# Kernel tuning notes

Measured on AMD Instinct MI355X. Metric: run time of the kernel, lower is better.

Reference implementation:

```python
import jax, jax.numpy as jnp
import numpy as np

D_MODEL = 1024
N_HEADS = 16
D_HEAD = 64
NUM_REL_POS = 2047
B = 8
L = 1024


def setup_inputs() -> dict:
    key = jax.random.key(0)
    ks = jax.random.split(key, 8)
    s = 1.0 / np.sqrt(D_MODEL)
    x = jax.random.normal(ks[0], (B, L, D_MODEL), dtype=jnp.float32)
    rel_indices = jax.random.randint(ks[1], (L, L), 0, NUM_REL_POS)
    Wq = jax.random.normal(ks[2], (D_MODEL, D_MODEL), dtype=jnp.float32) * s
    Wk = jax.random.normal(ks[3], (D_MODEL, D_MODEL), dtype=jnp.float32) * s
    Wv = jax.random.normal(ks[4], (D_MODEL, D_MODEL), dtype=jnp.float32) * s
    Wo = jax.random.normal(ks[5], (D_MODEL, D_MODEL), dtype=jnp.float32) * s
    rel_k = jax.random.normal(ks[6], (NUM_REL_POS, D_HEAD), dtype=jnp.float32) * 0.02
    rel_v = jax.random.normal(ks[7], (NUM_REL_POS, D_HEAD), dtype=jnp.float32) * 0.02
    return {"x": x, "rel_indices": rel_indices, "Wq": Wq, "Wk": Wk,
            "Wv": Wv, "Wo": Wo, "rel_k": rel_k, "rel_v": rel_v}


def reference(x, rel_indices, Wq, Wk, Wv, Wo, rel_k, rel_v):
    Bz, Ls, D = x.shape
    H, dk = N_HEADS, D_HEAD
    scale = 1.0 / np.sqrt(dk)
    # torch Linear: y = x @ W.T, weights are [out, in]
    q = jnp.einsum('bld,ed->ble', x, Wq).reshape(Bz, Ls, H, dk).transpose(0, 2, 1, 3)
    k = jnp.einsum('bld,ed->ble', x, Wk).reshape(Bz, Ls, H, dk).transpose(0, 2, 1, 3)
    v = jnp.einsum('bld,ed->ble', x, Wv).reshape(Bz, Ls, H, dk).transpose(0, 2, 1, 3)
    r_k = rel_k[rel_indices]  # (L, L, dk)
    r_v = rel_v[rel_indices]  # (L, L, dk)
    content = jnp.einsum('bhid,bhjd->bhij', q, k)
    rel = jnp.einsum('bhid,ijd->bhij', q, r_k)
    scores = (content + rel) * scale
    probs = jax.nn.softmax(scores, axis=-1)  # dropout = 0 (eval)
    out = jnp.einsum('bhij,bhjd->bhid', probs, v) + jnp.einsum('bhij,ijd->bhid', probs, r_v)
    out = out.transpose(0, 2, 1, 3).reshape(Bz, Ls, D)
    return jnp.einsum('bld,ed->ble', out, Wo)
```

## Files before the change

kernel.cpp:

```cpp
#include <hip/hip_runtime.h>

#define B_ 8
#define H_ 16
#define L_ 1024
#define DH_ 64
#define DM_ 1024
#define NP_ 2047
#define NP2_ 2048
#define SCALE_ 0.125f

#define PS_ 1032
#define HS_ 260

typedef __attribute__((ext_vector_type(8))) short bf16x8;
typedef __attribute__((ext_vector_type(4))) float f32x4;

__device__ __forceinline__ unsigned short f2bf(float x) {
    union { float f; unsigned int u; } v; v.f = x;
    return (unsigned short)((v.u + 0x7FFFu + ((v.u >> 16) & 1u)) >> 16);
}
__device__ __forceinline__ float bf2f(unsigned short b) {
    union { unsigned int u; float f; } v; v.u = ((unsigned int)b) << 16;
    return v.f;
}

template <int MODE>
__global__ __launch_bounds__(256) void proj_gemm(const float* __restrict__ X,
                                                 const float* __restrict__ W,
                                                 float* __restrict__ Yf,
                                                 unsigned short* __restrict__ Y0,
                                                 unsigned short* __restrict__ Y1)
{
    __shared__ __align__(16) float As[16][132];
    __shared__ __align__(16) float Bs[16][132];
    const int t   = threadIdx.x;
    const int tm  = t & 15;
    const int tn  = t >> 4;
    const int row0 = blockIdx.x * 128;
    const int col0 = blockIdx.y * 128;
    const int lr  = t >> 1;
    const int lc  = (t & 1) * 8;

    float acc[8][8];
#pragma unroll
    for (int i = 0; i < 8; ++i)
#pragma unroll
        for (int j = 0; j < 8; ++j) acc[i][j] = 0.f;

    float4 xa, xb, wa, wb;
    const float* xp = X + (size_t)(row0 + lr) * DM_ + lc;
    const float* wp = W + (size_t)(col0 + lr) * DM_ + lc;
    xa = *(const float4*)(xp);     xb = *(const float4*)(xp + 4);
    wa = *(const float4*)(wp);     wb = *(const float4*)(wp + 4);

    for (int k0 = 0; k0 < DM_; k0 += 16) {
        __syncthreads();
        As[lc + 0][lr] = xa.x; As[lc + 1][lr] = xa.y; As[lc + 2][lr] = xa.z; As[lc + 3][lr] = xa.w;
        As[lc + 4][lr] = xb.x; As[lc + 5][lr] = xb.y; As[lc + 6][lr] = xb.z; As[lc + 7][lr] = xb.w;
        Bs[lc + 0][lr] = wa.x; Bs[lc + 1][lr] = wa.y; Bs[lc + 2][lr] = wa.z; Bs[lc + 3][lr] = wa.w;
        Bs[lc + 4][lr] = wb.x; Bs[lc + 5][lr] = wb.y; Bs[lc + 6][lr] = wb.z; Bs[lc + 7][lr] = wb.w;
        __syncthreads();
        if (k0 + 16 < DM_) {
            xa = *(const float4*)(xp + k0 + 16);  xb = *(const float4*)(xp + k0 + 20);
            wa = *(const float4*)(wp + k0 + 16);  wb = *(const float4*)(wp + k0 + 20);
        }
#pragma unroll
        for (int kk = 0; kk < 16; ++kk) {
            float4 a0 = *(const float4*)&As[kk][tm * 4];
            float4 a1 = *(const float4*)&As[kk][64 + tm * 4];
            float4 b0 = *(const float4*)&Bs[kk][tn * 8];
            float4 b1 = *(const float4*)&Bs[kk][tn * 8 + 4];
            const float av[8] = {a0.x, a0.y, a0.z, a0.w, a1.x, a1.y, a1.z, a1.w};
            const float bv[8] = {b0.x, b0.y, b0.z, b0.w, b1.x, b1.y, b1.z, b1.w};
#pragma unroll
            for (int i = 0; i < 8; ++i)
#pragma unroll
                for (int j = 0; j < 8; ++j)
                    acc[i][j] = fmaf(av[i], bv[j], acc[i][j]);
        }
    }

    const int bidx = row0 >> 10;
    const int hbase = blockIdx.y * 2 + (tn >> 3);
    const int dbase = (tn & 7) * 8;

    if constexpr (MODE == 1) {
#pragma unroll
        for (int i = 0; i < 8; ++i) {
            const int row = row0 + ((i < 4) ? (tm * 4 + i) : (64 + tm * 4 + i - 4));
            *(float4*)(Yf + (size_t)row * DM_ + col0 + tn * 8)     = make_float4(acc[i][0], acc[i][1], acc[i][2], acc[i][3]);
            *(float4*)(Yf + (size_t)row * DM_ + col0 + tn * 8 + 4) = make_float4(acc[i][4], acc[i][5], acc[i][6], acc[i][7]);
        }
    }
    if constexpr (MODE == 0) {
#pragma unroll
        for (int i = 0; i < 8; ++i) {
            const int row = row0 + ((i < 4) ? (tm * 4 + i) : (64 + tm * 4 + i - 4));
            const int l = row & 1023;
            const size_t base = (((size_t)bidx * H_ + hbase) * L_ + l) * DH_ + dbase;
#pragma unroll
            for (int jh = 0; jh < 2; ++jh) {
                ushort4 hi4, lo4;
                unsigned short* hp = (unsigned short*)&hi4;
                unsigned short* lp = (unsigned short*)&lo4;
#pragma unroll
                for (int j = 0; j < 4; ++j) {
                    const float y = acc[i][jh * 4 + j];
                    unsigned short hb = f2bf(y);
                    hp[j] = hb;
                    lp[j] = f2bf(y - bf2f(hb));
                }
                *(ushort4*)(Y0 + base + jh * 4) = hi4;
                *(ushort4*)(Y1 + base + jh * 4) = lo4;
            }
        }
    }
    if constexpr (MODE == 2) {
#pragma unroll
        for (int j = 0; j < 8; ++j) {
            const int d = dbase + j;
            const size_t cb = ((size_t)(bidx * H_ + hbase) * DH_ + d) * L_;
#pragma unroll
            for (int half = 0; half < 2; ++half) {
                const int l0 = (row0 & 1023) + half * 64 + tm * 4;
                ushort4 v4;
                unsigned short* vp = (unsigned short*)&v4;
#pragma unroll
                for (int i = 0; i < 4; ++i) vp[i] = f2bf(acc[half * 4 + i][j]);
                *(ushort4*)(Y0 + cb + l0) = v4;
            }
        }
    }
}

__global__ __launch_bounds__(256) void prep_rel(const float* __restrict__ rk,
                                                const float* __restrict__ rv,
                                                unsigned short* __restrict__ rk_hi,
                                                unsigned short* __restrict__ rv_t)
{
    const int idx = blockIdx.x * 256 + threadIdx.x;
    const int p = idx >> 6;
    const int d = idx & 63;
    float xk = (p < NP_) ? rk[(size_t)p * DH_ + d] : 0.f;
    rk_hi[idx] = f2bf(xk);
    float xv = (p < NP_) ? rv[(size_t)p * DH_ + d] : 0.f;
    rv_t[(size_t)d * NP2_ + p] = f2bf(xv);
}

__global__ __launch_bounds__(512, 4) void shaw_attn_mfma(
    const unsigned short* __restrict__ qh, const unsigned short* __restrict__ ql,
    const unsigned short* __restrict__ kh, const unsigned short* __restrict__ kl,
    const unsigned short* __restrict__ vt, const int* __restrict__ ridx,
    const unsigned short* __restrict__ rkh, const unsigned short* __restrict__ rvt,
    float* __restrict__ out)
{
    __shared__ __align__(16) unsigned char regionA[16 * PS_ * 2];
    __shared__ __align__(16) unsigned char regionB[16 * HS_ * 4];
    __shared__ float pmax[16][8];
    __shared__ float psum[16][8];

    char*           qrel8 = (char*)regionA;
    unsigned short* Pu    = (unsigned short*)regionA;
    float*          hist  = (float*)regionB;
    float*          red   = (float*)regionB;

    const int t    = threadIdx.x;
    const int w    = t >> 6;
    const int lane = t & 63;
    const int mrow = lane & 15;
    const int grp  = lane >> 4;
    const int i0   = blockIdx.x * 16;
    const int h    = blockIdx.y;
    const int b    = blockIdx.z;
    const size_t bh = (size_t)b * H_ + h;

    const unsigned short* qhp = qh + bh * (size_t)(L_ * DH_);
    const unsigned short* qlp = ql + bh * (size_t)(L_ * DH_);
    const unsigned short* khp = kh + bh * (size_t)(L_ * DH_);
    const unsigned short* klp = kl + bh * (size_t)(L_ * DH_);
    const unsigned short* vtp = vt + bh * (size_t)(DH_ * L_);

    bf16x8 qAh[2], qAl[2];
#pragma unroll
    for (int s = 0; s < 2; ++s) {
        const size_t off = (size_t)(i0 + mrow) * DH_ + s * 32 + grp * 8;
        qAh[s] = *(const bf16x8*)(qhp + off);
        qAl[s] = *(const bf16x8*)(qlp + off);
    }

    {
        const unsigned short* rb = rkh + (size_t)(w * 256 + mrow) * DH_ + grp * 8;
#pragma unroll 4
        for (int tt = 0; tt < 16; ++tt) {
            bf16x8 Bh0 = *(const bf16x8*)(rb + tt * 1024);
            bf16x8 Bh1 = *(const bf16x8*)(rb + tt * 1024 + 32);
            f32x4 c = {0.f, 0.f, 0.f, 0.f};
            c = __builtin_amdgcn_mfma_f32_16x16x32_bf16(qAh[0], Bh0, c, 0, 0, 0);
            c = __builtin_amdgcn_mfma_f32_16x16x32_bf16(qAh[1], Bh1, c, 0, 0, 0);
            const int pcol = (w * 16 + tt) * 16 + mrow;
            unsigned int pk = 0;
#pragma unroll
            for (int r = 0; r < 4; ++r) {
                int qi = (int)rintf(c[r] * 128.f);
                qi = qi > 127 ? 127 : (qi < -127 ? -127 : qi);
                pk |= ((unsigned int)(qi & 0xff)) << (8 * r);
            }
            *(unsigned int*)(qrel8 + pcol * 16 + grp * 4) = pk;
        }
    }
    __syncthreads();

    float sc[8][4];
    {
        const unsigned short* kbh = khp + (size_t)(w * 128 + mrow) * DH_ + grp * 8;
        const unsigned short* kbl = klp + (size_t)(w * 128 + mrow) * DH_ + grp * 8;
#pragma unroll 2
        for (int tt = 0; tt < 8; ++tt) {
            bf16x8 Bh0 = *(const bf16x8*)(kbh + tt * 1024);
            bf16x8 Bh1 = *(const bf16x8*)(kbh + tt * 1024 + 32);
            bf16x8 Bl0 = *(const bf16x8*)(kbl + tt * 1024);
            bf16x8 Bl1 = *(const bf16x8*)(kbl + tt * 1024 + 32);
            f32x4 c = {0.f, 0.f, 0.f, 0.f};
            c = __builtin_amdgcn_mfma_f32_16x16x32_bf16(qAh[0], Bh0, c, 0, 0, 0);
            c = __builtin_amdgcn_mfma_f32_16x16x32_bf16(qAh[1], Bh1, c, 0, 0, 0);
            c = __builtin_amdgcn_mfma_f32_16x16x32_bf16(qAh[0], Bl0, c, 0, 0, 0);
            c = __builtin_amdgcn_mfma_f32_16x16x32_bf16(qAh[1], Bl1, c, 0, 0, 0);
            c = __builtin_amdgcn_mfma_f32_16x16x32_bf16(qAl[0], Bh0, c, 0, 0, 0);
            c = __builtin_amdgcn_mfma_f32_16x16x32_bf16(qAl[1], Bh1, c, 0, 0, 0);
#pragma unroll
            for (int r = 0; r < 4; ++r) sc[tt][r] = c[r] * SCALE_;
        }
    }

    unsigned int pidxPk[16];
#pragma unroll
    for (int tt = 0; tt < 8; ++tt) {
        const int jcol = (w * 8 + tt) * 16 + mrow;
        unsigned int pk0 = 0, pk1 = 0;
#pragma unroll
        for (int r = 0; r < 4; ++r) {
            const int pidx = ridx[(size_t)(i0 + grp * 4 + r) * L_ + jcol];
            sc[tt][r] = fmaf((float)qrel8[pidx * 16 + grp * 4 + r], SCALE_ / 128.f, sc[tt][r]);
            if (r < 2) pk0 |= ((unsigned int)pidx) << (16 * r);
            else       pk1 |= ((unsigned int)pidx) << (16 * (r - 2));
        }
        pidxPk[tt * 2]     = pk0;
        pidxPk[tt * 2 + 1] = pk1;
    }

    float mx[4];
#pragma unroll
    for (int r = 0; r < 4; ++r) {
        float m = sc[0][r];
#pragma unroll
        for (int tt = 1; tt < 8; ++tt) m = fmaxf(m, sc[tt][r]);
#pragma unroll
        for (int off = 1; off < 16; off <<= 1) m = fmaxf(m, __shfl_xor(m, off));
        mx[r] = m;
    }
    {
        const float wv0 = (mrow == 0) ? mx[0] : (mrow == 1) ? mx[1] : (mrow == 2) ? mx[2] : mx[3];
        if (mrow < 4) pmax[grp * 4 + mrow][w] = wv0;
    }
    __syncthreads();

    float gm[4];
#pragma unroll
    for (int r = 0; r < 4; ++r) {
        const int rr = grp * 4 + r;
        float m = pmax[rr][0];
#pragma unroll
        for (int u = 1; u < 8; ++u) m = fmaxf(m, pmax[rr][u]);
        gm[r] = m;
    }
    float sm[4] = {0.f, 0.f, 0.f, 0.f};
#pragma unroll
    for (int tt = 0; tt < 8; ++tt) {
        const int jcol = (w * 8 + tt) * 16 + mrow;
#pragma unroll
        for (int r = 0; r < 4; ++r) {
            const float e = __expf(sc[tt][r] - gm[r]);
            sm[r] += e;
            Pu[(grp * 4 + r) * PS_ + jcol] = f2bf(e);
        }
    }
#pragma unroll
    for (int r = 0; r < 4; ++r) {
#pragma unroll
        for (int off = 1; off < 16; off <<= 1) sm[r] += __shfl_xor(sm[r], off);
    }
    {
        const float sv0 = (mrow == 0) ? sm[0] : (mrow == 1) ? sm[1] : (mrow == 2) ? sm[2] : sm[3];
        if (mrow < 4) psum[grp * 4 + mrow][w] = sv0;
    }
    __syncthreads();

    const int n = w & 3;
    const int khalf = w >> 2;
    f32x4 acc = {0.f, 0.f, 0.f, 0.f};
    {
        const unsigned short* vcol = vtp + (size_t)(n * 16 + mrow) * L_ + khalf * 512 + grp * 8;
#pragma unroll 4
        for (int s = 0; s < 16; ++s) {
            bf16x8 a  = *(const bf16x8*)(Pu + mrow * PS_ + khalf * 512 + s * 32 + grp * 8);
            bf16x8 bb = *(const bf16x8*)(vcol + s * 32);
            acc = __builtin_amdgcn_mfma_f32_16x16x32_bf16(a, bb, acc, 0, 0, 0);
        }
    }

    for (int pass = 0; pass < 8; ++pass) {
        {
            float4* h4 = (float4*)hist;
            const float4 z4 = make_float4(0.f, 0.f, 0.f, 0.f);
            for (int z = t; z < (16 * HS_) / 4; z += 512) h4[z] = z4;
        }
        __syncthreads();
#pragma unroll
        for (int tt = 0; tt < 8; ++tt) {
            const int jcol = (w * 8 + tt) * 16 + mrow;
#pragma unroll
            for (int rp = 0; rp < 2; ++rp) {
                const unsigned int pk = pidxPk[tt * 2 + rp];
#pragma unroll
                for (int j = 0; j < 2; ++j) {
                    const int r  = rp * 2 + j;
                    const int rr = grp * 4 + r;
                    const int pidx = (int)((pk >> (16 * j)) & 0xffffu);
                    if ((pidx >> 8) == pass)
                        atomicAdd(&hist[rr * HS_ + (pidx & 255)], bf2f(Pu[rr * PS_ + jcol]));
                }
            }
        }
        __syncthreads();
        const unsigned short* rvcol =
            rvt + (size_t)(n * 16 + mrow) * NP2_ + pass * 256 + khalf * 128 + grp * 8;
#pragma unroll
        for (int s = 0; s < 4; ++s) {
            const int kb = khalf * 128 + s * 32;
            const f32x4* hp = (const f32x4*)&hist[mrow * HS_ + kb + grp * 8];
            f32x4 h0 = hp[0], h1 = hp[1];
            bf16x8 a;
#pragma unroll
            for (int e = 0; e < 4; ++e) { a[e] = (short)f2bf(h0[e]); a[e + 4] = (short)f2bf(h1[e]); }
            bf16x8 bb = *(const bf16x8*)(rvcol + s * 32);
            acc = __builtin_amdgcn_mfma_f32_16x16x32_bf16(a, bb, acc, 0, 0, 0);
        }
        __syncthreads();
    }

#pragma unroll
    for (int r = 0; r < 4; ++r) red[w * 320 + (grp * 4 + r) * 20 + mrow] = acc[r];
    __syncthreads();
    if (w < 4) {
#pragma unroll
        for (int r = 0; r < 4; ++r) {
            const int rr = grp * 4 + r;
            float o = red[w * 320 + rr * 20 + mrow] + red[(w + 4) * 320 + rr * 20 + mrow];
            float ssum = 0.f;
#pragma unroll
            for (int u = 0; u < 8; ++u) ssum += psum[rr][u];
            out[((size_t)b * L_ + i0 + rr) * DM_ + h * DH_ + w * 16 + mrow] = o / ssum;
        }
    }
}

extern "C" void kernel_launch(void* const* d_in, const int* in_sizes, int n_in,
                              void* d_out, int out_size, void* d_ws, size_t ws_size,
                              hipStream_t stream)
{
    const float* x    = (const float*)d_in[0];
    const int*   ridx = (const int*)  d_in[1];
    const float* Wq   = (const float*)d_in[2];
    const float* Wk   = (const float*)d_in[3];
    const float* Wv   = (const float*)d_in[4];
    const float* Wo   = (const float*)d_in[5];
    const float* rk   = (const float*)d_in[6];
    const float* rv   = (const float*)d_in[7];
    float* out = (float*)d_out;

    const size_t NQ = (size_t)B_ * H_ * L_ * DH_;
    float* attn = (float*)d_ws;
    unsigned short* u = (unsigned short*)(attn + NQ);
    unsigned short* qh = u;            u += NQ;
    unsigned short* ql = u;            u += NQ;
    unsigned short* kh = u;            u += NQ;
    unsigned short* kl = u;            u += NQ;
    unsigned short* vt = u;            u += NQ;
    unsigned short* rkh = u;           u += (size_t)NP2_ * DH_;
    unsigned short* rvt = u;           u += (size_t)NP2_ * DH_;

    dim3 gthr(256);
    dim3 ggrid((B_ * L_) / 128, DM_ / 128);

    prep_rel<<<dim3((NP2_ * DH_) / 256), gthr, 0, stream>>>(rk, rv, rkh, rvt);
    proj_gemm<0><<<ggrid, gthr, 0, stream>>>(x, Wq, nullptr, qh, ql);
    proj_gemm<0><<<ggrid, gthr, 0, stream>>>(x, Wk, nullptr, kh, kl);
    proj_gemm<2><<<ggrid, gthr, 0, stream>>>(x, Wv, nullptr, vt, nullptr);

    shaw_attn_mfma<<<dim3(L_ / 16, H_, B_), dim3(512), 0, stream>>>(
        qh, ql, kh, kl, vt, ridx, rkh, rvt, attn);

    proj_gemm<1><<<ggrid, gthr, 0, stream>>>(attn, Wo, out, nullptr, nullptr);
}
```

Baseline: 2.143 ms.

## Double-buffer histogram in LDS and prefetch rel_v tiles across passes

Splits the per-pass histogram into two LDS buffers so the next buffer is zeroed while the current one is consumed, which removes one __syncthreads per pass. It also prefetches the next pass's rel_v fragments into registers ahead of the MFMA loop to hide global load latency. The cost is doubled regionB LDS usage and more live registers, which may reduce occupancy under the 512-thread launch bound of 4 blocks.

```diff
diff --git a/kernel.cpp b/kernel.cpp
--- a/kernel.cpp
+++ b/kernel.cpp
@@ -155,13 +155,14 @@
     float* __restrict__ out)
 {
     __shared__ __align__(16) unsigned char regionA[16 * PS_ * 2];
-    __shared__ __align__(16) unsigned char regionB[16 * HS_ * 4];
+    __shared__ __align__(16) unsigned char regionB[2 * 16 * HS_ * 4];
     __shared__ float pmax[16][8];
     __shared__ float psum[16][8];
 
     char*           qrel8 = (char*)regionA;
     unsigned short* Pu    = (unsigned short*)regionA;
-    float*          hist  = (float*)regionB;
+    float*          histA = (float*)regionB;
+    float*          histB = histA + 16 * HS_;
     float*          red   = (float*)regionB;
 
     const int t    = threadIdx.x;
@@ -293,6 +294,11 @@
         const float sv0 = (mrow == 0) ? sm[0] : (mrow == 1) ? sm[1] : (mrow == 2) ? sm[2] : sm[3];
         if (mrow < 4) psum[grp * 4 + mrow][w] = sv0;
     }
+    {
+        float4* h4 = (float4*)histA;
+        const float4 z4 = make_float4(0.f, 0.f, 0.f, 0.f);
+        for (int z = t; z < (16 * HS_) / 4; z += 512) h4[z] = z4;
+    }
     __syncthreads();
 
     const int n = w & 3;
@@ -308,13 +314,14 @@
         }
     }
 
+    const unsigned short* rvbase = rvt + (size_t)(n * 16 + mrow) * NP2_ + khalf * 128 + grp * 8;
+    bf16x8 rvf[4];
+#pragma unroll
+    for (int s = 0; s < 4; ++s) rvf[s] = *(const bf16x8*)(rvbase + s * 32);
+
     for (int pass = 0; pass < 8; ++pass) {
-        {
-            float4* h4 = (float4*)hist;
-            const float4 z4 = make_float4(0.f, 0.f, 0.f, 0.f);
-            for (int z = t; z < (16 * HS_) / 4; z += 512) h4[z] = z4;
-        }
-        __syncthreads();
+        float* cur = (pass & 1) ? histB : histA;
+        float* nxt = (pass & 1) ? histA : histB;
 #pragma unroll
         for (int tt = 0; tt < 8; ++tt) {
             const int jcol = (w * 8 + tt) * 16 + mrow;
@@ -327,23 +334,33 @@
                     const int rr = grp * 4 + r;
                     const int pidx = (int)((pk >> (16 * j)) & 0xffffu);
                     if ((pidx >> 8) == pass)
-                        atomicAdd(&hist[rr * HS_ + (pidx & 255)], bf2f(Pu[rr * PS_ + jcol]));
+                        atomicAdd(&cur[rr * HS_ + (pidx & 255)], bf2f(Pu[rr * PS_ + jcol]));
                 }
             }
         }
         __syncthreads();
-        const unsigned short* rvcol =
-            rvt + (size_t)(n * 16 + mrow) * NP2_ + pass * 256 + khalf * 128 + grp * 8;
+
+        bf16x8 rvn[4];
+        if (pass + 1 < 8) {
+#pragma unroll
+            for (int s = 0; s < 4; ++s) rvn[s] = *(const bf16x8*)(rvbase + (pass + 1) * 256 + s * 32);
+        }
 #pragma unroll
         for (int s = 0; s < 4; ++s) {
             const int kb = khalf * 128 + s * 32;
-            const f32x4* hp = (const f32x4*)&hist[mrow * HS_ + kb + grp * 8];
+            const f32x4* hp = (const f32x4*)&cur[mrow * HS_ + kb + grp * 8];
             f32x4 h0 = hp[0], h1 = hp[1];
             bf16x8 a;
 #pragma unroll
             for (int e = 0; e < 4; ++e) { a[e] = (short)f2bf(h0[e]); a[e + 4] = (short)f2bf(h1[e]); }
-            bf16x8 bb = *(const bf16x8*)(rvcol + s * 32);
-            acc = __builtin_amdgcn_mfma_f32_16x16x32_bf16(a, bb, acc, 0, 0, 0);
+            acc = __builtin_amdgcn_mfma_f32_16x16x32_bf16(a, rvf[s], acc, 0, 0, 0);
+        }
+        if (pass + 1 < 8) {
+            float4* h4 = (float4*)nxt;
+            const float4 z4 = make_float4(0.f, 0.f, 0.f, 0.f);
+            for (int z = t; z < (16 * HS_) / 4; z += 512) h4[z] = z4;
+#pragma unroll
+            for (int s = 0; s < 4; ++s) rvf[s] = rvn[s];
         }
         __syncthreads();
     }
```

New measurement: 2.323 ms. 1.08x slower.
